# Performance work log

Hardware: AMD Instinct MI355X
Metric: run time of the kernel (lower is better)

Reference implementation:

```python
import math
import jax, jax.numpy as jnp
import numpy as np

B, T, D = 512, 512, 256
ALPHA = 0.5
BETA = 0.9


def setup_inputs() -> dict:
    key = jax.random.key(0)
    ks = jax.random.split(key, 9)
    s = 1.0 / math.sqrt(D)
    return {
        "window_features": jax.random.normal(ks[0], (B, T, D), jnp.float32),
        "timestamps": jax.random.uniform(ks[1], (B, T), jnp.float32) * 86400.0 * 7,
        "prev_L": jax.random.normal(ks[2], (B, D), jnp.float32),
        "prev_M": jax.random.uniform(ks[3], (B, 1), jnp.float32),
        "pad_mask": jnp.zeros((B, T), jnp.bool_),
        "W_Q": jax.random.normal(ks[4], (D, D), jnp.float32) * s,
        "W_K": jax.random.normal(ks[5], (D, D), jnp.float32) * s,
        "W_V": jax.random.normal(ks[6], (D, D), jnp.float32) * s,
        "cls_w": jax.random.normal(ks[7], (1, 2 * D + 1), jnp.float32) * s,
        "cls_b": jnp.zeros((1,), jnp.float32),
    }


def reference(window_features, timestamps, prev_L, prev_M, pad_mask,
              W_Q, W_K, W_V, cls_w, cls_b):
    Bv, Tv, d = window_features.shape
    valid = ~pad_mask
    valid_f = valid.astype(window_features.dtype)              # [B,T]
    valid_count = jnp.clip(valid_f.sum(1, keepdims=True), 1.0)  # [B,1]

    # decay weights from recency (days)
    t_masked = jnp.where(pad_mask, -1e18, timestamps)
    t_max = t_masked.max(1, keepdims=True)                      # [B,1]
    dt = jnp.clip(t_max - timestamps, 0.0) / 86400.0
    lam = jnp.exp(-ALPHA * dt) * valid_f                        # [B,T]

    # mean-pooled query
    q = (window_features * valid_f[..., None]).sum(1) / valid_count  # [B,d]
    Q = q @ W_Q.T                                               # [B,d]
    K = jnp.einsum('btd,ed->bte', window_features, W_K)         # [B,T,d]
    V = jnp.einsum('btd,ed->bte', window_features, W_V)         # [B,T,d]

    scores = jnp.einsum('bd,btd->bt', Q, K) / math.sqrt(d)      # [B,T]
    scores = jnp.where(pad_mask, -1e9, scores)
    attn = jax.nn.softmax(scores, axis=-1)

    # decay-modulated reweighting + renormalization
    w = lam * attn
    w = w / (w.sum(1, keepdims=True) + 1e-8)

    L_t = jnp.einsum('bt,btd->bd', w, V)                        # [B,d]
    delta_t = L_t - prev_L
    M_t = BETA * prev_M + (1.0 - BETA) * jnp.linalg.norm(delta_t, axis=1, keepdims=True)
    T_event = jnp.concatenate([L_t, delta_t, M_t], axis=-1)     # [B,2d+1]
    p = (T_event @ cls_w.T + cls_b).squeeze(-1)                 # [B]
    return (p, T_event, L_t, M_t)
```

## Files before the change

### kernel.cpp

```cpp
#include <hip/hip_runtime.h>
#include <math.h>

#define ALPHA 0.5f
#define BETA 0.9f
#define Bsz 512
#define Tsz 512
#define Dsz 256

__device__ __forceinline__ float wave_reduce_sum(float v) {
    v += __shfl_xor(v, 32, 64);
    v += __shfl_xor(v, 16, 64);
    v += __shfl_xor(v, 8, 64);
    v += __shfl_xor(v, 4, 64);
    v += __shfl_xor(v, 2, 64);
    v += __shfl_xor(v, 1, 64);
    return v;
}

__device__ __forceinline__ float wave_reduce_max(float v) {
    v = fmaxf(v, __shfl_xor(v, 32, 64));
    v = fmaxf(v, __shfl_xor(v, 16, 64));
    v = fmaxf(v, __shfl_xor(v, 8, 64));
    v = fmaxf(v, __shfl_xor(v, 4, 64));
    v = fmaxf(v, __shfl_xor(v, 2, 64));
    v = fmaxf(v, __shfl_xor(v, 1, 64));
    return v;
}

__global__ __launch_bounds__(256) void kA(const float* __restrict__ x,
                                          const float* __restrict__ ts,
                                          const unsigned char* __restrict__ pad,
                                          const float* __restrict__ WQ,
                                          const float* __restrict__ WK,
                                          float* __restrict__ qk,
                                          float* __restrict__ tmax_out) {
    const int b = blockIdx.x;
    const int tid = threadIdx.x;
    const int w = tid >> 6, lane = tid & 63;

    __shared__ float validS[Tsz];
    __shared__ float qpart[4][Dsz];
    __shared__ float qS[Dsz];
    __shared__ float QS[Dsz];
    __shared__ float red[8];
    __shared__ float tmaxS, cntS;

    float lmax = -1e30f;
    float lcnt = 0.f;
    for (int t = tid; t < Tsz; t += 256) {
        bool v = (pad[(size_t)b * Tsz + t] == 0);
        float tv = ts[(size_t)b * Tsz + t];
        validS[t] = v ? 1.f : 0.f;
        if (v) { lmax = fmaxf(lmax, tv); lcnt += 1.f; }
    }
    lmax = wave_reduce_max(lmax);
    lcnt = wave_reduce_sum(lcnt);
    if (lane == 0) { red[w] = lmax; red[4 + w] = lcnt; }
    __syncthreads();
    if (tid == 0) {
        tmaxS = fmaxf(fmaxf(red[0], red[1]), fmaxf(red[2], red[3]));
        cntS = fmaxf(red[4] + red[5] + red[6] + red[7], 1.f);
    }
    __syncthreads();

    const float* xb = x + (size_t)b * Tsz * Dsz;
    float4 a0 = make_float4(0.f, 0.f, 0.f, 0.f);
    float4 a1 = a0, a2 = a0, a3 = a0;
    const int tbase = w * 128;
    for (int i = 0; i < 128; i += 4) {
        const int t = tbase + i;
        float4 x0 = *(const float4*)(xb + (size_t)(t + 0) * Dsz + lane * 4);
        float4 x1 = *(const float4*)(xb + (size_t)(t + 1) * Dsz + lane * 4);
        float4 x2 = *(const float4*)(xb + (size_t)(t + 2) * Dsz + lane * 4);
        float4 x3 = *(const float4*)(xb + (size_t)(t + 3) * Dsz + lane * 4);
        const float v0 = validS[t], v1 = validS[t + 1], v2 = validS[t + 2], v3 = validS[t + 3];
        a0.x += v0 * x0.x; a0.y += v0 * x0.y; a0.z += v0 * x0.z; a0.w += v0 * x0.w;
        a1.x += v1 * x1.x; a1.y += v1 * x1.y; a1.z += v1 * x1.z; a1.w += v1 * x1.w;
        a2.x += v2 * x2.x; a2.y += v2 * x2.y; a2.z += v2 * x2.z; a2.w += v2 * x2.w;
        a3.x += v3 * x3.x; a3.y += v3 * x3.y; a3.z += v3 * x3.z; a3.w += v3 * x3.w;
    }
    float4 accq;
    accq.x = (a0.x + a1.x) + (a2.x + a3.x);
    accq.y = (a0.y + a1.y) + (a2.y + a3.y);
    accq.z = (a0.z + a1.z) + (a2.z + a3.z);
    accq.w = (a0.w + a1.w) + (a2.w + a3.w);
    qpart[w][lane * 4 + 0] = accq.x;
    qpart[w][lane * 4 + 1] = accq.y;
    qpart[w][lane * 4 + 2] = accq.z;
    qpart[w][lane * 4 + 3] = accq.w;
    __syncthreads();
    qS[tid] = (qpart[0][tid] + qpart[1][tid] + qpart[2][tid] + qpart[3][tid]) / cntS;
    __syncthreads();

    float Qi = 0.f;
    const float* wqrow = WQ + (size_t)tid * Dsz;
    #pragma unroll 4
    for (int d4 = 0; d4 < Dsz; d4 += 4) {
        float4 wv = *(const float4*)(wqrow + d4);
        Qi += wv.x * qS[d4] + wv.y * qS[d4 + 1] + wv.z * qS[d4 + 2] + wv.w * qS[d4 + 3];
    }
    QS[tid] = Qi;
    __syncthreads();

    float v = 0.f;
    #pragma unroll 8
    for (int e = 0; e < Dsz; ++e) {
        v += QS[e] * WK[(size_t)e * Dsz + tid];
    }
    qk[(size_t)b * Dsz + tid] = v * 0.0625f;
    if (tid == 0) tmax_out[b] = tmaxS;
}

__global__ __launch_bounds__(256) void kB(const float* __restrict__ x,
                                          const float* __restrict__ ts,
                                          const unsigned char* __restrict__ pad,
                                          const float* __restrict__ qk,
                                          const float* __restrict__ tmax_in,
                                          const float* __restrict__ WV,
                                          const float* __restrict__ prevL,
                                          const float* __restrict__ prevM,
                                          const float* __restrict__ clsw,
                                          const float* __restrict__ clsb,
                                          float* __restrict__ out) {
    const int b = blockIdx.x;
    const int tid = threadIdx.x;
    const int w = tid >> 6, lane = tid & 63;

    __shared__ float lamS[Tsz];
    __shared__ float okS[Tsz];
    __shared__ float accS[4][Dsz];
    __shared__ float EGS[8];
    __shared__ float xwS[Dsz];
    __shared__ float red[4];
    __shared__ float red2[4];

    const float tmax = tmax_in[b];
    for (int t = tid; t < Tsz; t += 256) {
        bool valid = (pad[(size_t)b * Tsz + t] == 0);
        float dt = fmaxf(tmax - ts[(size_t)b * Tsz + t], 0.f) * (1.f / 86400.f);
        lamS[t] = valid ? __expf(-ALPHA * dt) : 0.f;
        okS[t] = valid ? 1.f : 0.f;
    }
    __syncthreads();

    const float4 qk4 = *(const float4*)(qk + (size_t)b * Dsz + lane * 4);
    const float* xb = x + (size_t)b * Tsz * Dsz;
    float4 acc = make_float4(0.f, 0.f, 0.f, 0.f);
    float E = 0.f, G = 0.f;
    const int tbase = w * 128;
    for (int i = 0; i < 128; i += 4) {
        const int t = tbase + i;
        float4 x0 = *(const float4*)(xb + (size_t)(t + 0) * Dsz + lane * 4);
        float4 x1 = *(const float4*)(xb + (size_t)(t + 1) * Dsz + lane * 4);
        float4 x2 = *(const float4*)(xb + (size_t)(t + 2) * Dsz + lane * 4);
        float4 x3 = *(const float4*)(xb + (size_t)(t + 3) * Dsz + lane * 4);
        float s0 = qk4.x * x0.x + qk4.y * x0.y + qk4.z * x0.z + qk4.w * x0.w;
        float s1 = qk4.x * x1.x + qk4.y * x1.y + qk4.z * x1.z + qk4.w * x1.w;
        float s2 = qk4.x * x2.x + qk4.y * x2.y + qk4.z * x2.z + qk4.w * x2.w;
        float s3 = qk4.x * x3.x + qk4.y * x3.y + qk4.z * x3.z + qk4.w * x3.w;
        #pragma unroll
        for (int off = 32; off >= 1; off >>= 1) {
            s0 += __shfl_xor(s0, off, 64);
            s1 += __shfl_xor(s1, off, 64);
            s2 += __shfl_xor(s2, off, 64);
            s3 += __shfl_xor(s3, off, 64);
        }
        float e0 = okS[t + 0] * __expf(s0);
        float e1 = okS[t + 1] * __expf(s1);
        float e2 = okS[t + 2] * __expf(s2);
        float e3 = okS[t + 3] * __expf(s3);
        float g0 = lamS[t + 0] * e0;
        float g1 = lamS[t + 1] * e1;
        float g2 = lamS[t + 2] * e2;
        float g3 = lamS[t + 3] * e3;
        E += (e0 + e1) + (e2 + e3);
        G += (g0 + g1) + (g2 + g3);
        acc.x += g0 * x0.x + g1 * x1.x + g2 * x2.x + g3 * x3.x;
        acc.y += g0 * x0.y + g1 * x1.y + g2 * x2.y + g3 * x3.y;
        acc.z += g0 * x0.z + g1 * x1.z + g2 * x2.z + g3 * x3.z;
        acc.w += g0 * x0.w + g1 * x1.w + g2 * x2.w + g3 * x3.w;
    }
    accS[w][lane * 4 + 0] = acc.x;
    accS[w][lane * 4 + 1] = acc.y;
    accS[w][lane * 4 + 2] = acc.z;
    accS[w][lane * 4 + 3] = acc.w;
    if (lane == 0) { EGS[w] = E; EGS[4 + w] = G; }
    __syncthreads();

    {
        float Et = EGS[0] + EGS[1] + EGS[2] + EGS[3];
        float Gt = EGS[4] + EGS[5] + EGS[6] + EGS[7];
        float denom = Gt + 1e-8f * Et;
        float accd = accS[0][tid] + accS[1][tid] + accS[2][tid] + accS[3][tid];
        xwS[tid] = (denom > 0.f) ? accd / denom : 0.f;
    }
    __syncthreads();

    float Le = 0.f;
    const float* wvrow = WV + (size_t)tid * Dsz;
    #pragma unroll 4
    for (int d4 = 0; d4 < Dsz; d4 += 4) {
        float4 wv = *(const float4*)(wvrow + d4);
        Le += wv.x * xwS[d4] + wv.y * xwS[d4 + 1] + wv.z * xwS[d4 + 2] + wv.w * xwS[d4 + 3];
    }
    float delta = Le - prevL[(size_t)b * Dsz + tid];

    float ssq = wave_reduce_sum(delta * delta);
    if (lane == 0) red[w] = ssq;
    __syncthreads();
    float nrm = sqrtf(red[0] + red[1] + red[2] + red[3]);
    float M = BETA * prevM[b] + (1.f - BETA) * nrm;

    float pp = Le * clsw[tid] + delta * clsw[Dsz + tid];
    float psum = wave_reduce_sum(pp);
    if (lane == 0) red2[w] = psum;
    __syncthreads();

    float* out_p = out;
    float* out_T = out + Bsz;
    float* out_L = out + Bsz + (size_t)Bsz * (2 * Dsz + 1);
    float* out_M = out + Bsz + (size_t)Bsz * (2 * Dsz + 1) + (size_t)Bsz * Dsz;

    out_T[(size_t)b * (2 * Dsz + 1) + tid] = Le;
    out_T[(size_t)b * (2 * Dsz + 1) + Dsz + tid] = delta;
    out_L[(size_t)b * Dsz + tid] = Le;
    if (tid == 0) {
        float p = red2[0] + red2[1] + red2[2] + red2[3] + M * clsw[2 * Dsz] + clsb[0];
        out_p[b] = p;
        out_T[(size_t)b * (2 * Dsz + 1) + 2 * Dsz] = M;
        out_M[b] = M;
    }
}

extern "C" void kernel_launch(void* const* d_in, const int* in_sizes, int n_in,
                              void* d_out, int out_size, void* d_ws, size_t ws_size,
                              hipStream_t stream) {
    const float* x     = (const float*)d_in[0];
    const float* ts    = (const float*)d_in[1];
    const float* prevL = (const float*)d_in[2];
    const float* prevM = (const float*)d_in[3];
    const unsigned char* pad = (const unsigned char*)d_in[4];
    const float* WQ    = (const float*)d_in[5];
    const float* WK    = (const float*)d_in[6];
    const float* WV    = (const float*)d_in[7];
    const float* clsw  = (const float*)d_in[8];
    const float* clsb  = (const float*)d_in[9];

    float* ws   = (float*)d_ws;
    float* qk   = ws;
    float* tmax = ws + Bsz * Dsz;

    kA<<<Bsz, 256, 0, stream>>>(x, ts, pad, WQ, WK, qk, tmax);
    kB<<<Bsz, 256, 0, stream>>>(x, ts, pad, qk, tmax, WV, prevL, prevM, clsw, clsb, (float*)d_out);
}
```

Measured before the change: 453.3 us.

## Split sequence dimension into chunks across blocks with separate reduction kernels

Splits each batch row's T=512 sequence into 4 chunks processed by separate blocks, producing partial sums of the pooled query, softmax-weighted accumulators and normalizers in workspace. Two small follow-up kernels combine the partials and perform the D×D projections and output epilogue. This raises the number of blocks streaming the large input to improve memory-level parallelism, at the cost of extra launches and workspace traffic.

Result: no change. 458.8 us (+1.2%).

```diff
diff --git a/kernel.cpp b/kernel.cpp
--- a/kernel.cpp
+++ b/kernel.cpp
@@ -6,6 +6,8 @@
 #define Bsz 512
 #define Tsz 512
 #define Dsz 256
+#define NCHUNK 4
+#define CROWS (Tsz / NCHUNK)
 
 __device__ __forceinline__ float wave_reduce_sum(float v) {
     v += __shfl_xor(v, 32, 64);
@@ -27,69 +29,85 @@
     return v;
 }
 
-__global__ __launch_bounds__(256) void kA(const float* __restrict__ x,
-                                          const float* __restrict__ ts,
-                                          const unsigned char* __restrict__ pad,
-                                          const float* __restrict__ WQ,
-                                          const float* __restrict__ WK,
-                                          float* __restrict__ qk,
-                                          float* __restrict__ tmax_out) {
-    const int b = blockIdx.x;
+__global__ __launch_bounds__(256) void kA1(const float* __restrict__ x,
+                                           const float* __restrict__ ts,
+                                           const unsigned char* __restrict__ pad,
+                                           float* __restrict__ qpart,
+                                           float* __restrict__ cntp,
+                                           float* __restrict__ tmaxp) {
+    const int idx = blockIdx.x;
+    const int b = idx >> 2, chunk = idx & 3;
     const int tid = threadIdx.x;
     const int w = tid >> 6, lane = tid & 63;
-
-    __shared__ float validS[Tsz];
-    __shared__ float qpart[4][Dsz];
-    __shared__ float qS[Dsz];
-    __shared__ float QS[Dsz];
+    const int t0 = chunk * CROWS;
+
+    __shared__ float validS[CROWS];
+    __shared__ float part[4][Dsz];
     __shared__ float red[8];
-    __shared__ float tmaxS, cntS;
-
-    float lmax = -1e30f;
-    float lcnt = 0.f;
-    for (int t = tid; t < Tsz; t += 256) {
-        bool v = (pad[(size_t)b * Tsz + t] == 0);
-        float tv = ts[(size_t)b * Tsz + t];
-        validS[t] = v ? 1.f : 0.f;
-        if (v) { lmax = fmaxf(lmax, tv); lcnt += 1.f; }
+
+    float lmax = -3e38f, lcnt = 0.f;
+    if (tid < CROWS) {
+        bool v = (pad[(size_t)b * Tsz + t0 + tid] == 0);
+        float tv = ts[(size_t)b * Tsz + t0 + tid];
+        validS[tid] = v ? 1.f : 0.f;
+        if (v) { lmax = tv; lcnt = 1.f; }
     }
     lmax = wave_reduce_max(lmax);
     lcnt = wave_reduce_sum(lcnt);
     if (lane == 0) { red[w] = lmax; red[4 + w] = lcnt; }
     __syncthreads();
-    if (tid == 0) {
-        tmaxS = fmaxf(fmaxf(red[0], red[1]), fmaxf(red[2], red[3]));
-        cntS = fmaxf(red[4] + red[5] + red[6] + red[7], 1.f);
-    }
-    __syncthreads();
 
     const float* xb = x + (size_t)b * Tsz * Dsz;
     float4 a0 = make_float4(0.f, 0.f, 0.f, 0.f);
     float4 a1 = a0, a2 = a0, a3 = a0;
-    const int tbase = w * 128;
-    for (int i = 0; i < 128; i += 4) {
-        const int t = tbase + i;
-        float4 x0 = *(const float4*)(xb + (size_t)(t + 0) * Dsz + lane * 4);
-        float4 x1 = *(const float4*)(xb + (size_t)(t + 1) * Dsz + lane * 4);
-        float4 x2 = *(const float4*)(xb + (size_t)(t + 2) * Dsz + lane * 4);
-        float4 x3 = *(const float4*)(xb + (size_t)(t + 3) * Dsz + lane * 4);
-        const float v0 = validS[t], v1 = validS[t + 1], v2 = validS[t + 2], v3 = validS[t + 3];
+    const int lb = w * 32;
+    for (int i = 0; i < 32; i += 4) {
+        const int lt = lb + i;
+        const size_t g = (size_t)(t0 + lt) * Dsz + lane * 4;
+        float4 x0 = *(const float4*)(xb + g);
+        float4 x1 = *(const float4*)(xb + g + Dsz);
+        float4 x2 = *(const float4*)(xb + g + 2 * Dsz);
+        float4 x3 = *(const float4*)(xb + g + 3 * Dsz);
+        const float v0 = validS[lt], v1 = validS[lt + 1], v2 = validS[lt + 2], v3 = validS[lt + 3];
         a0.x += v0 * x0.x; a0.y += v0 * x0.y; a0.z += v0 * x0.z; a0.w += v0 * x0.w;
         a1.x += v1 * x1.x; a1.y += v1 * x1.y; a1.z += v1 * x1.z; a1.w += v1 * x1.w;
         a2.x += v2 * x2.x; a2.y += v2 * x2.y; a2.z += v2 * x2.z; a2.w += v2 * x2.w;
         a3.x += v3 * x3.x; a3.y += v3 * x3.y; a3.z += v3 * x3.z; a3.w += v3 * x3.w;
     }
-    float4 accq;
-    accq.x = (a0.x + a1.x) + (a2.x + a3.x);
-    accq.y = (a0.y + a1.y) + (a2.y + a3.y);
-    accq.z = (a0.z + a1.z) + (a2.z + a3.z);
-    accq.w = (a0.w + a1.w) + (a2.w + a3.w);
-    qpart[w][lane * 4 + 0] = accq.x;
-    qpart[w][lane * 4 + 1] = accq.y;
-    qpart[w][lane * 4 + 2] = accq.z;
-    qpart[w][lane * 4 + 3] = accq.w;
-    __syncthreads();
-    qS[tid] = (qpart[0][tid] + qpart[1][tid] + qpart[2][tid] + qpart[3][tid]) / cntS;
+    part[w][lane * 4 + 0] = (a0.x + a1.x) + (a2.x + a3.x);
+    part[w][lane * 4 + 1] = (a0.y + a1.y) + (a2.y + a3.y);
+    part[w][lane * 4 + 2] = (a0.z + a1.z) + (a2.z + a3.z);
+    part[w][lane * 4 + 3] = (a0.w + a1.w) + (a2.w + a3.w);
+    __syncthreads();
+    qpart[(size_t)idx * Dsz + tid] = (part[0][tid] + part[1][tid]) + (part[2][tid] + part[3][tid]);
+    if (tid == 0) {
+        tmaxp[idx] = fmaxf(fmaxf(red[0], red[1]), fmaxf(red[2], red[3]));
+        cntp[idx] = (red[4] + red[5]) + (red[6] + red[7]);
+    }
+}
+
+__global__ __launch_bounds__(256) void kA2(const float* __restrict__ qpart,
+                                           const float* __restrict__ cntp,
+                                           const float* __restrict__ tmaxp,
+                                           const float* __restrict__ WQ,
+                                           const float* __restrict__ WK,
+                                           float* __restrict__ qk,
+                                           float* __restrict__ tmax_out) {
+    const int b = blockIdx.x;
+    const int tid = threadIdx.x;
+    __shared__ float qS[Dsz];
+    __shared__ float QS[Dsz];
+    __shared__ float cntS;
+
+    if (tid == 0) {
+        float tm = fmaxf(fmaxf(tmaxp[b * 4], tmaxp[b * 4 + 1]),
+                         fmaxf(tmaxp[b * 4 + 2], tmaxp[b * 4 + 3]));
+        cntS = fmaxf(cntp[b * 4] + cntp[b * 4 + 1] + cntp[b * 4 + 2] + cntp[b * 4 + 3], 1.f);
+        tmax_out[b] = tm;
+    }
+    __syncthreads();
+    qS[tid] = ((qpart[(size_t)(b * 4 + 0) * Dsz + tid] + qpart[(size_t)(b * 4 + 1) * Dsz + tid]) +
+               (qpart[(size_t)(b * 4 + 2) * Dsz + tid] + qpart[(size_t)(b * 4 + 3) * Dsz + tid])) / cntS;
     __syncthreads();
 
     float Qi = 0.f;
@@ -108,38 +126,33 @@
         v += QS[e] * WK[(size_t)e * Dsz + tid];
     }
     qk[(size_t)b * Dsz + tid] = v * 0.0625f;
-    if (tid == 0) tmax_out[b] = tmaxS;
-}
-
-__global__ __launch_bounds__(256) void kB(const float* __restrict__ x,
-                                          const float* __restrict__ ts,
-                                          const unsigned char* __restrict__ pad,
-                                          const float* __restrict__ qk,
-                                          const float* __restrict__ tmax_in,
-                                          const float* __restrict__ WV,
-                                          const float* __restrict__ prevL,
-                                          const float* __restrict__ prevM,
-                                          const float* __restrict__ clsw,
-                                          const float* __restrict__ clsb,
-                                          float* __restrict__ out) {
-    const int b = blockIdx.x;
+}
+
+__global__ __launch_bounds__(256) void kB1(const float* __restrict__ x,
+                                           const float* __restrict__ ts,
+                                           const unsigned char* __restrict__ pad,
+                                           const float* __restrict__ qk,
+                                           const float* __restrict__ tmax_in,
+                                           float* __restrict__ accp,
+                                           float* __restrict__ Ep,
+                                           float* __restrict__ Gp) {
+    const int idx = blockIdx.x;
+    const int b = idx >> 2, chunk = idx & 3;
     const int tid = threadIdx.x;
     const int w = tid >> 6, lane = tid & 63;
-
-    __shared__ float lamS[Tsz];
-    __shared__ float okS[Tsz];
+    const int t0 = chunk * CROWS;
+
+    __shared__ float lamS[CROWS];
+    __shared__ float okS[CROWS];
     __shared__ float accS[4][Dsz];
     __shared__ float EGS[8];
-    __shared__ float xwS[Dsz];
-    __shared__ float red[4];
-    __shared__ float red2[4];
 
     const float tmax = tmax_in[b];
-    for (int t = tid; t < Tsz; t += 256) {
-        bool valid = (pad[(size_t)b * Tsz + t] == 0);
-        float dt = fmaxf(tmax - ts[(size_t)b * Tsz + t], 0.f) * (1.f / 86400.f);
-        lamS[t] = valid ? __expf(-ALPHA * dt) : 0.f;
-        okS[t] = valid ? 1.f : 0.f;
+    if (tid < CROWS) {
+        bool valid = (pad[(size_t)b * Tsz + t0 + tid] == 0);
+        float dt = fmaxf(tmax - ts[(size_t)b * Tsz + t0 + tid], 0.f) * (1.f / 86400.f);
+        lamS[tid] = valid ? __expf(-ALPHA * dt) : 0.f;
+        okS[tid] = valid ? 1.f : 0.f;
     }
     __syncthreads();
 
@@ -147,13 +160,14 @@
     const float* xb = x + (size_t)b * Tsz * Dsz;
     float4 acc = make_float4(0.f, 0.f, 0.f, 0.f);
     float E = 0.f, G = 0.f;
-    const int tbase = w * 128;
-    for (int i = 0; i < 128; i += 4) {
-        const int t = tbase + i;
-        float4 x0 = *(const float4*)(xb + (size_t)(t + 0) * Dsz + lane * 4);
-        float4 x1 = *(const float4*)(xb + (size_t)(t + 1) * Dsz + lane * 4);
-        float4 x2 = *(const float4*)(xb + (size_t)(t + 2) * Dsz + lane * 4);
-        float4 x3 = *(const float4*)(xb + (size_t)(t + 3) * Dsz + lane * 4);
+    const int lb = w * 32;
+    for (int i = 0; i < 32; i += 4) {
+        const int lt = lb + i;
+        const size_t g = (size_t)(t0 + lt) * Dsz + lane * 4;
+        float4 x0 = *(const float4*)(xb + g);
+        float4 x1 = *(const float4*)(xb + g + Dsz);
+        float4 x2 = *(const float4*)(xb + g + 2 * Dsz);
+        float4 x3 = *(const float4*)(xb + g + 3 * Dsz);
         float s0 = qk4.x * x0.x + qk4.y * x0.y + qk4.z * x0.z + qk4.w * x0.w;
         float s1 = qk4.x * x1.x + qk4.y * x1.y + qk4.z * x1.z + qk4.w * x1.w;
         float s2 = qk4.x * x2.x + qk4.y * x2.y + qk4.z * x2.z + qk4.w * x2.w;
@@ -165,14 +179,14 @@
             s2 += __shfl_xor(s2, off, 64);
             s3 += __shfl_xor(s3, off, 64);
         }
-        float e0 = okS[t + 0] * __expf(s0);
-        float e1 = okS[t + 1] * __expf(s1);
-        float e2 = okS[t + 2] * __expf(s2);
-        float e3 = okS[t + 3] * __expf(s3);
-        float g0 = lamS[t + 0] * e0;
-        float g1 = lamS[t + 1] * e1;
-        float g2 = lamS[t + 2] * e2;
-        float g3 = lamS[t + 3] * e3;
+        float e0 = okS[lt + 0] * __expf(s0);
+        float e1 = okS[lt + 1] * __expf(s1);
+        float e2 = okS[lt + 2] * __expf(s2);
+        float e3 = okS[lt + 3] * __expf(s3);
+        float g0 = lamS[lt + 0] * e0;
+        float g1 = lamS[lt + 1] * e1;
+        float g2 = lamS[lt + 2] * e2;
+        float g3 = lamS[lt + 3] * e3;
         E += (e0 + e1) + (e2 + e3);
         G += (g0 + g1) + (g2 + g3);
         acc.x += g0 * x0.x + g1 * x1.x + g2 * x2.x + g3 * x3.x;
@@ -186,14 +200,36 @@
     accS[w][lane * 4 + 3] = acc.w;
     if (lane == 0) { EGS[w] = E; EGS[4 + w] = G; }
     __syncthreads();
-
-    {
-        float Et = EGS[0] + EGS[1] + EGS[2] + EGS[3];
-        float Gt = EGS[4] + EGS[5] + EGS[6] + EGS[7];
-        float denom = Gt + 1e-8f * Et;
-        float accd = accS[0][tid] + accS[1][tid] + accS[2][tid] + accS[3][tid];
-        xwS[tid] = (denom > 0.f) ? accd / denom : 0.f;
-    }
+    accp[(size_t)idx * Dsz + tid] = (accS[0][tid] + accS[1][tid]) + (accS[2][tid] + accS[3][tid]);
+    if (tid == 0) {
+        Ep[idx] = (EGS[0] + EGS[1]) + (EGS[2] + EGS[3]);
+        Gp[idx] = (EGS[4] + EGS[5]) + (EGS[6] + EGS[7]);
+    }
+}
+
+__global__ __launch_bounds__(256) void kB2(const float* __restrict__ accp,
+                                           const float* __restrict__ Ep,
+                                           const float* __restrict__ Gp,
+                                           const float* __restrict__ WV,
+                                           const float* __restrict__ prevL,
+                                           const float* __restrict__ prevM,
+                                           const float* __restrict__ clsw,
+                                           const float* __restrict__ clsb,
+                                           float* __restrict__ out) {
+    const int b = blockIdx.x;
+    const int tid = threadIdx.x;
+    const int w = tid >> 6, lane = tid & 63;
+
+    __shared__ float xwS[Dsz];
+    __shared__ float red[4];
+    __shared__ float red2[4];
+
+    float E = (Ep[b * 4] + Ep[b * 4 + 1]) + (Ep[b * 4 + 2] + Ep[b * 4 + 3]);
+    float G = (Gp[b * 4] + Gp[b * 4 + 1]) + (Gp[b * 4 + 2] + Gp[b * 4 + 3]);
+    float denom = G + 1e-8f * E;
+    float accd = (accp[(size_t)(b * 4 + 0) * Dsz + tid] + accp[(size_t)(b * 4 + 1) * Dsz + tid]) +
+                 (accp[(size_t)(b * 4 + 2) * Dsz + tid] + accp[(size_t)(b * 4 + 3) * Dsz + tid]);
+    xwS[tid] = (denom > 0.f) ? accd / denom : 0.f;
     __syncthreads();
 
     float Le = 0.f;
@@ -208,7 +244,7 @@
     float ssq = wave_reduce_sum(delta * delta);
     if (lane == 0) red[w] = ssq;
     __syncthreads();
-    float nrm = sqrtf(red[0] + red[1] + red[2] + red[3]);
+    float nrm = sqrtf((red[0] + red[1]) + (red[2] + red[3]));
     float M = BETA * prevM[b] + (1.f - BETA) * nrm;
 
     float pp = Le * clsw[tid] + delta * clsw[Dsz + tid];
@@ -225,7 +261,7 @@
     out_T[(size_t)b * (2 * Dsz + 1) + Dsz + tid] = delta;
     out_L[(size_t)b * Dsz + tid] = Le;
     if (tid == 0) {
-        float p = red2[0] + red2[1] + red2[2] + red2[3] + M * clsw[2 * Dsz] + clsb[0];
+        float p = (red2[0] + red2[1]) + (red2[2] + red2[3]) + M * clsw[2 * Dsz] + clsb[0];
         out_p[b] = p;
         out_T[(size_t)b * (2 * Dsz + 1) + 2 * Dsz] = M;
         out_M[b] = M;
@@ -246,10 +282,18 @@
     const float* clsw  = (const float*)d_in[8];
     const float* clsb  = (const float*)d_in[9];
 
-    float* ws   = (float*)d_ws;
-    float* qk   = ws;
-    float* tmax = ws + Bsz * Dsz;
-
-    kA<<<Bsz, 256, 0, stream>>>(x, ts, pad, WQ, WK, qk, tmax);
-    kB<<<Bsz, 256, 0, stream>>>(x, ts, pad, qk, tmax, WV, prevL, prevM, clsw, clsb, (float*)d_out);
-}
+    float* ws = (float*)d_ws;
+    float* qk    = ws;
+    float* tmax  = qk + (size_t)Bsz * Dsz;
+    float* qpart = tmax + Bsz;
+    float* cntp  = qpart + (size_t)Bsz * NCHUNK * Dsz;
+    float* tmaxp = cntp + (size_t)Bsz * NCHUNK;
+    float* accp  = tmaxp + (size_t)Bsz * NCHUNK;
+    float* Ep    = accp + (size_t)Bsz * NCHUNK * Dsz;
+    float* Gp    = Ep + (size_t)Bsz * NCHUNK;
+
+    kA1<<<Bsz * NCHUNK, 256, 0, stream>>>(x, ts, pad, qpart, cntp, tmaxp);
+    kA2<<<Bsz, 256, 0, stream>>>(qpart, cntp, tmaxp, WQ, WK, qk, tmax);
+    kB1<<<Bsz * NCHUNK, 256, 0, stream>>>(x, ts, pad, qk, tmax, accp, Ep, Gp);
+    kB2<<<Bsz, 256, 0, stream>>>(accp, Ep, Gp, WV, prevL, prevM, clsw, clsb, (float*)d_out);
+}
```
